# Optimization experiments

Measured on AMD Instinct MI355X. Metric: run time of the kernel, lower is better.

The kernel has to match this reference:

```python
import jax, jax.numpy as jnp
import numpy as np

N = 50000      # nodes
E = 800000     # edges
DIN = 128      # in_channels
H = 128        # hidden_channels
G = 64         # graphs in batch
OUT = 8        # head out_channels


def setup_inputs() -> dict:
    key = jax.random.key(0)
    ks = jax.random.split(key, 12)
    s = 0.1  # weight init scale
    x = jax.random.normal(ks[0], (N, DIN), jnp.float32)
    edge_index = jax.random.randint(ks[1], (2, E), 0, N, dtype=jnp.int64)
    batch = jnp.sort(jax.random.randint(ks[2], (N,), 0, G, dtype=jnp.int64))
    W0 = jax.random.normal(ks[3], (DIN, H), jnp.float32) * s
    b0 = jnp.zeros((H,), jnp.float32)
    W1 = jax.random.normal(ks[4], (H, H), jnp.float32) * s
    b1 = jnp.zeros((H,), jnp.float32)
    W2 = jax.random.normal(ks[5], (H, H), jnp.float32) * s
    b2 = jnp.zeros((H,), jnp.float32)
    Wh = jax.random.normal(ks[6], (H, OUT), jnp.float32) * s
    bh = jnp.zeros((OUT,), jnp.float32)
    return {"x": x, "edge_index": edge_index, "batch": batch,
            "W0": W0, "b0": b0, "W1": W1, "b1": b1, "W2": W2, "b2": b2,
            "Wh": Wh, "bh": bh}


def gcn_conv(x, src, dst, W, b):
    # GCNConv with self-loops and symmetric normalization (PyG defaults).
    h = x @ W                                           # [N, H]
    deg = jnp.zeros((N,), h.dtype).at[dst].add(1.0) + 1.0   # in-degree incl. self-loop
    dinv = jax.lax.rsqrt(deg)                           # deg^{-1/2}
    coef = dinv[src] * dinv[dst]                        # [E]
    agg = jnp.zeros_like(h).at[dst].add(h[src] * coef[:, None])
    # self-loop contribution: dinv[i]^2 * h[i]
    return agg + h * (dinv * dinv)[:, None] + b


def reference(x, edge_index, batch, W0, b0, W1, b1, W2, b2, Wh, bh):
    src, dst = edge_index[0], edge_index[1]
    h = jax.nn.relu(gcn_conv(x, src, dst, W0, b0))
    h = jax.nn.relu(gcn_conv(h, src, dst, W1, b1))
    h = gcn_conv(h, src, dst, W2, b2)                   # last layer: no activation
    # global mean pool over graphs
    sums = jnp.zeros((G, H), h.dtype).at[batch].add(h)
    cnt = jnp.zeros((G,), h.dtype).at[batch].add(1.0)
    pooled = sums / jnp.maximum(cnt, 1.0)[:, None]      # [G, H]
    return pooled @ Wh + bh                             # [G, OUT]
```

## Files before the change

kernel.cpp:

```cpp
#include <hip/hip_runtime.h>

#define N_NODES 50000
#define N_EDGES 800000
#define HD 128
#define NGRAPH 64
#define NOUT 8
#define SLOTS 64

typedef __attribute__((ext_vector_type(8))) short bf8_t;
typedef __attribute__((ext_vector_type(4))) float f4_t;
typedef __attribute__((ext_vector_type(8))) unsigned short us8;

__device__ __forceinline__ unsigned short f2b(float f) {
    unsigned u = __float_as_uint(f);
    u += 0x7fffu + ((u >> 16) & 1u);
    return (unsigned short)(u >> 16);
}
__device__ __forceinline__ float b2f(unsigned short h) {
    return __uint_as_float(((unsigned)h) << 16);
}

__global__ __launch_bounds__(256) void fill1_k(const int* __restrict__ src,
                                               const int* __restrict__ dst,
                                               int* __restrict__ degc,
                                               unsigned short* __restrict__ slots) {
    int e = blockIdx.x * 256 + threadIdx.x;
    if (e >= N_EDGES) return;
    int s = __builtin_nontemporal_load(src + e);
    int d = __builtin_nontemporal_load(dst + e);
    int pos = atomicAdd(&degc[d], 1);
    if (pos < SLOTS)
        slots[(size_t)d * SLOTS + pos] = (unsigned short)s;
}

__global__ __launch_bounds__(256) void cvtw_k(const float* __restrict__ W0,
                                              const float* __restrict__ W1,
                                              const float* __restrict__ W2,
                                              unsigned short* __restrict__ WT) {
    int idx = blockIdx.x * 256 + threadIdx.x;
    if (idx >= 3 * HD * HD) return;
    int w = idx >> 14;
    int rem = idx & 16383;
    int n = rem >> 7;
    int k = rem & 127;
    const float* W = (w == 0) ? W0 : (w == 1) ? W1 : W2;
    WT[(size_t)w * HD * HD + n * HD + k] = f2b(W[k * HD + n]);
}

__global__ __launch_bounds__(256) void mm_f32in_k(const float* __restrict__ X,
                                                  const unsigned short* __restrict__ WT,
                                                  const int* __restrict__ degc,
                                                  unsigned short* __restrict__ Y) {
    const int lane = threadIdx.x & 63;
    const int wave = threadIdx.x >> 6;
    const int r = lane & 15;
    const int q = lane >> 4;
    const int row0 = blockIdx.x * 64 + wave * 16;
    int arow = row0 + r; if (arow >= N_NODES) arow = N_NODES - 1;

    f4_t acc[8];
#pragma unroll
    for (int n = 0; n < 8; ++n) acc[n] = (f4_t){0.f, 0.f, 0.f, 0.f};

#pragma unroll
    for (int kb = 0; kb < 4; ++kb) {
        float4 fa = *(const float4*)(X + (size_t)arow * HD + kb * 32 + q * 8);
        float4 fb = *(const float4*)(X + (size_t)arow * HD + kb * 32 + q * 8 + 4);
        bf8_t a;
        a[0] = (short)f2b(fa.x); a[1] = (short)f2b(fa.y);
        a[2] = (short)f2b(fa.z); a[3] = (short)f2b(fa.w);
        a[4] = (short)f2b(fb.x); a[5] = (short)f2b(fb.y);
        a[6] = (short)f2b(fb.z); a[7] = (short)f2b(fb.w);
#pragma unroll
        for (int n = 0; n < 8; ++n) {
            bf8_t b = *(const bf8_t*)(WT + (size_t)(n * 16 + r) * HD + kb * 32 + q * 8);
            acc[n] = __builtin_amdgcn_mfma_f32_16x16x32_bf16(a, b, acc[n], 0, 0, 0);
        }
    }
    const int orow = row0 + q * 4;
#pragma unroll
    for (int i = 0; i < 4; ++i) {
        int rr = orow + i;
        if (rr < N_NODES) {
            float dv = rsqrtf((float)degc[rr] + 1.0f);
#pragma unroll
            for (int n = 0; n < 8; ++n)
                Y[(size_t)rr * HD + n * 16 + r] = f2b(acc[n][i] * dv);
        }
    }
}

__global__ __launch_bounds__(256) void fusedGM2_k(const unsigned short* __restrict__ T,
                                                  const int* __restrict__ degc,
                                                  const unsigned short* __restrict__ slots,
                                                  const float* __restrict__ bias,
                                                  const unsigned short* __restrict__ WT,
                                                  unsigned short* __restrict__ Y) {
    __shared__ unsigned short hs[16][136];
    const int tid = threadIdx.x;
    const int base = blockIdx.x * 16;

    {
        const int g = tid >> 4;
        const int l = tid & 15;
        const int j8 = l * 8;
        const int i = base + g;
        const int dg = degc[i];
        int dc = dg; if (dc > SLOTS) dc = SLOTS;
        const float di = rsqrtf((float)dg + 1.0f);
        const unsigned short* sl = slots + (size_t)i * SLOTS;

        float a[8];
#pragma unroll
        for (int k = 0; k < 8; ++k) a[k] = 0.f;
        int e = 0;
        for (; e + 15 < dc; e += 16) {
            us8 i0 = *(const us8*)(sl + e);
            us8 i1 = *(const us8*)(sl + e + 8);
            us8 v[16];
#pragma unroll
            for (int u = 0; u < 8; ++u) v[u]     = *(const us8*)(T + (size_t)i0[u] * HD + j8);
#pragma unroll
            for (int u = 0; u < 8; ++u) v[u + 8] = *(const us8*)(T + (size_t)i1[u] * HD + j8);
#pragma unroll
            for (int u = 0; u < 16; ++u) {
#pragma unroll
                for (int k = 0; k < 8; ++k) a[k] += b2f(v[u][k]);
            }
        }
        if (e < dc) {
            us8 i0 = *(const us8*)(sl + e);
            us8 i1 = *(const us8*)(sl + e + 8);
            const unsigned short safe = i0[0];
            int s[16]; float m[16];
#pragma unroll
            for (int u = 0; u < 8; ++u) {
                m[u] = (e + u < dc) ? 1.f : 0.f;
                s[u] = (e + u < dc) ? i0[u] : safe;
            }
#pragma unroll
            for (int u = 0; u < 8; ++u) {
                m[u + 8] = (e + 8 + u < dc) ? 1.f : 0.f;
                s[u + 8] = (e + 8 + u < dc) ? i1[u] : safe;
            }
            us8 v[16];
#pragma unroll
            for (int u = 0; u < 16; ++u) v[u] = *(const us8*)(T + (size_t)s[u] * HD + j8);
#pragma unroll
            for (int u = 0; u < 16; ++u) {
#pragma unroll
                for (int k = 0; k < 8; ++k) a[k] = fmaf(m[u], b2f(v[u][k]), a[k]);
            }
        }
        us8 tv = *(const us8*)(T + (size_t)i * HD + j8);
        float4 bv0 = *(const float4*)(bias + j8);
        float4 bv1 = *(const float4*)(bias + j8 + 4);
        float bb[8] = {bv0.x, bv0.y, bv0.z, bv0.w, bv1.x, bv1.y, bv1.z, bv1.w};
        us8 o;
#pragma unroll
        for (int k = 0; k < 8; ++k) {
            float r = di * (a[k] + b2f(tv[k])) + bb[k];
            r = fmaxf(r, 0.f);
            o[k] = f2b(r);
        }
        *(us8*)(&hs[g][j8]) = o;
    }
    __syncthreads();

    {
        const int lane = tid & 63;
        const int wave = tid >> 6;
        const int r = lane & 15;
        const int q = lane >> 4;
        const int n0 = wave * 2;

        f4_t acc0 = (f4_t){0.f, 0.f, 0.f, 0.f};
        f4_t acc1 = (f4_t){0.f, 0.f, 0.f, 0.f};
#pragma unroll
        for (int kb = 0; kb < 4; ++kb) {
            bf8_t a = *(const bf8_t*)(&hs[r][kb * 32 + q * 8]);
            bf8_t b0 = *(const bf8_t*)(WT + (size_t)(n0 * 16 + r) * HD + kb * 32 + q * 8);
            bf8_t b1 = *(const bf8_t*)(WT + (size_t)(n0 * 16 + 16 + r) * HD + kb * 32 + q * 8);
            acc0 = __builtin_amdgcn_mfma_f32_16x16x32_bf16(a, b0, acc0, 0, 0, 0);
            acc1 = __builtin_amdgcn_mfma_f32_16x16x32_bf16(a, b1, acc1, 0, 0, 0);
        }
#pragma unroll
        for (int i = 0; i < 4; ++i) {
            int rr = base + q * 4 + i;
            float dv = rsqrtf((float)degc[rr] + 1.0f);
            Y[(size_t)rr * HD + n0 * 16 + r]      = f2b(acc0[i] * dv);
            Y[(size_t)rr * HD + n0 * 16 + 16 + r] = f2b(acc1[i] * dv);
        }
    }
}

__global__ __launch_bounds__(256) void gather_k(const unsigned short* __restrict__ T,
                                                const int* __restrict__ degc,
                                                const unsigned short* __restrict__ slots,
                                                const float* __restrict__ b,
                                                unsigned short* __restrict__ out) {
    int i = blockIdx.x * 16 + (threadIdx.x >> 4);
    if (i >= N_NODES) return;
    const int j8 = (threadIdx.x & 15) * 8;
    const int dg = degc[i];
    int dc = dg; if (dc > SLOTS) dc = SLOTS;
    const float di = rsqrtf((float)dg + 1.0f);
    const unsigned short* sl = slots + (size_t)i * SLOTS;

    float a[8];
#pragma unroll
    for (int k = 0; k < 8; ++k) a[k] = 0.f;
    int e = 0;
    for (; e + 15 < dc; e += 16) {
        us8 i0 = *(const us8*)(sl + e);
        us8 i1 = *(const us8*)(sl + e + 8);
        us8 v[16];
#pragma unroll
        for (int u = 0; u < 8; ++u) v[u]     = *(const us8*)(T + (size_t)i0[u] * HD + j8);
#pragma unroll
        for (int u = 0; u < 8; ++u) v[u + 8] = *(const us8*)(T + (size_t)i1[u] * HD + j8);
#pragma unroll
        for (int u = 0; u < 16; ++u) {
#pragma unroll
            for (int k = 0; k < 8; ++k) a[k] += b2f(v[u][k]);
        }
    }
    if (e < dc) {
        us8 i0 = *(const us8*)(sl + e);
        us8 i1 = *(const us8*)(sl + e + 8);
        const unsigned short safe = i0[0];
        int s[16]; float m[16];
#pragma unroll
        for (int u = 0; u < 8; ++u) {
            m[u] = (e + u < dc) ? 1.f : 0.f;
            s[u] = (e + u < dc) ? i0[u] : safe;
        }
#pragma unroll
        for (int u = 0; u < 8; ++u) {
            m[u + 8] = (e + 8 + u < dc) ? 1.f : 0.f;
            s[u + 8] = (e + 8 + u < dc) ? i1[u] : safe;
        }
        us8 v[16];
#pragma unroll
        for (int u = 0; u < 16; ++u) v[u] = *(const us8*)(T + (size_t)s[u] * HD + j8);
#pragma unroll
        for (int u = 0; u < 16; ++u) {
#pragma unroll
            for (int k = 0; k < 8; ++k) a[k] = fmaf(m[u], b2f(v[u][k]), a[k]);
        }
    }
    us8 tv = *(const us8*)(T + (size_t)i * HD + j8);
    float4 bv0 = *(const float4*)(b + j8);
    float4 bv1 = *(const float4*)(b + j8 + 4);
    float bb[8] = {bv0.x, bv0.y, bv0.z, bv0.w, bv1.x, bv1.y, bv1.z, bv1.w};
    us8 o;
#pragma unroll
    for (int k = 0; k < 8; ++k)
        o[k] = f2b(di * (a[k] + b2f(tv[k])) + bb[k]);
    *(us8*)(out + (size_t)i * HD + j8) = o;
}

__global__ __launch_bounds__(256) void pool2_k(const unsigned short* __restrict__ H2,
                                               const int* __restrict__ batch,
                                               float* __restrict__ sums,
                                               float* __restrict__ cnt) {
    const int t = threadIdx.x;
    const int f = t & 127;
    const int half = t >> 7;
    int i0 = blockIdx.x * 128 + half * 64;
    if (i0 >= N_NODES) return;
    int i1 = i0 + 64; if (i1 > N_NODES) i1 = N_NODES;

    int cur = batch[i0];
    float acc = 0.f;
    float c = 0.f;
    for (int i = i0; i < i1; ++i) {
        int g = batch[i];
        if (g != cur) {
            atomicAdd(&sums[cur * HD + f], acc);
            if (f == 0) atomicAdd(&cnt[cur], c);
            acc = 0.f; c = 0.f; cur = g;
        }
        acc += b2f(H2[(size_t)i * HD + f]);
        c += 1.f;
    }
    atomicAdd(&sums[cur * HD + f], acc);
    if (f == 0) atomicAdd(&cnt[cur], c);
}

__global__ __launch_bounds__(512) void head_k(const float* __restrict__ sums,
                                              const float* __restrict__ cnt,
                                              const float* __restrict__ Wh,
                                              const float* __restrict__ bh,
                                              float* __restrict__ out) {
    int t = threadIdx.x;
    int g = t >> 3, o = t & 7;
    float inv = 1.0f / fmaxf(cnt[g], 1.0f);
    float acc = bh[o];
    for (int h = 0; h < HD; ++h)
        acc += sums[g * HD + h] * inv * Wh[h * NOUT + o];
    out[g * NOUT + o] = acc;
}

extern "C" void kernel_launch(void* const* d_in, const int* in_sizes, int n_in,
                              void* d_out, int out_size, void* d_ws, size_t ws_size,
                              hipStream_t stream) {
    const float* x  = (const float*)d_in[0];
    const int*   ei = (const int*)d_in[1];
    const int*   batch = (const int*)d_in[2];
    const float* W0 = (const float*)d_in[3];
    const float* b0 = (const float*)d_in[4];
    const float* W1 = (const float*)d_in[5];
    const float* b1 = (const float*)d_in[6];
    const float* W2 = (const float*)d_in[7];
    const float* b2 = (const float*)d_in[8];
    const float* Wh = (const float*)d_in[9];
    const float* bh = (const float*)d_in[10];
    float* out = (float*)d_out;

    const int* src = ei;
    const int* dst = ei + N_EDGES;

    char* wsb = (char*)d_ws;
    int*            degc  = (int*)(wsb + 0);
    unsigned short* slots = (unsigned short*)(wsb + 200000);
    unsigned short* WT    = (unsigned short*)(wsb + 6600000);
    unsigned short* A     = (unsigned short*)(wsb + 6698304);
    unsigned short* C     = (unsigned short*)(wsb + 19498304);
    float*          sums  = (float*)(wsb + 32298304);
    float*          cnt   = (float*)(wsb + 32331072);

    const int mmGrid = (N_NODES + 63) / 64;
    const int gaGrid = (N_NODES + 15) / 16;

    hipMemsetAsync(degc, 0, N_NODES * sizeof(int), stream);
    fill1_k<<<(N_EDGES + 255) / 256, 256, 0, stream>>>(src, dst, degc, slots);
    cvtw_k<<<(3 * HD * HD + 255) / 256, 256, 0, stream>>>(W0, W1, W2, WT);

    mm_f32in_k<<<mmGrid, 256, 0, stream>>>(x, WT, degc, A);

    fusedGM2_k<<<gaGrid, 256, 0, stream>>>(A, degc, slots, b0, WT + HD * HD, C);

    fusedGM2_k<<<gaGrid, 256, 0, stream>>>(C, degc, slots, b1, WT + 2 * HD * HD, A);

    gather_k<<<gaGrid, 256, 0, stream>>>(A, degc, slots, b2, C);

    hipMemsetAsync(sums, 0, (NGRAPH * HD + NGRAPH) * sizeof(float), stream);
    pool2_k<<<(N_NODES + 127) / 128, 256, 0, stream>>>(C, batch, sums, cnt);
    head_k<<<1, 512, 0, stream>>>(sums, cnt, Wh, bh, out);
}
```

Measured before the change: 305.9 us.

## Merge edge fill with first matmul and fuse final gather with mean pooling

The first-layer matmul now writes unnormalized features, so it no longer depends on degrees and runs in the same launch as the edge-bucketing atomics. The first aggregation therefore applies per-neighbour normalization by reading degc for each neighbour. The last gather writes into shared memory and pools per block with atomics, which removes the write and re-read of the final hidden features and one launch. The cost is extra degc gathers and rsqrt work in layer one, plus more atomic traffic in pooling.

Measured after the change: 347.9 us. 1.14x slower.

```diff
diff --git a/kernel.cpp b/kernel.cpp
--- a/kernel.cpp
+++ b/kernel.cpp
@@ -6,6 +6,8 @@
 #define NGRAPH 64
 #define NOUT 8
 #define SLOTS 64
+#define MMGRID 782
+#define GAGRID 3125
 
 typedef __attribute__((ext_vector_type(8))) short bf8_t;
 typedef __attribute__((ext_vector_type(4))) float f4_t;
@@ -18,19 +20,6 @@
 }
 __device__ __forceinline__ float b2f(unsigned short h) {
     return __uint_as_float(((unsigned)h) << 16);
-}
-
-__global__ __launch_bounds__(256) void fill1_k(const int* __restrict__ src,
-                                               const int* __restrict__ dst,
-                                               int* __restrict__ degc,
-                                               unsigned short* __restrict__ slots) {
-    int e = blockIdx.x * 256 + threadIdx.x;
-    if (e >= N_EDGES) return;
-    int s = __builtin_nontemporal_load(src + e);
-    int d = __builtin_nontemporal_load(dst + e);
-    int pos = atomicAdd(&degc[d], 1);
-    if (pos < SLOTS)
-        slots[(size_t)d * SLOTS + pos] = (unsigned short)s;
 }
 
 __global__ __launch_bounds__(256) void cvtw_k(const float* __restrict__ W0,
@@ -47,45 +36,168 @@
     WT[(size_t)w * HD * HD + n * HD + k] = f2b(W[k * HD + n]);
 }
 
-__global__ __launch_bounds__(256) void mm_f32in_k(const float* __restrict__ X,
-                                                  const unsigned short* __restrict__ WT,
-                                                  const int* __restrict__ degc,
-                                                  unsigned short* __restrict__ Y) {
-    const int lane = threadIdx.x & 63;
-    const int wave = threadIdx.x >> 6;
-    const int r = lane & 15;
-    const int q = lane >> 4;
-    const int row0 = blockIdx.x * 64 + wave * 16;
-    int arow = row0 + r; if (arow >= N_NODES) arow = N_NODES - 1;
-
-    f4_t acc[8];
-#pragma unroll
-    for (int n = 0; n < 8; ++n) acc[n] = (f4_t){0.f, 0.f, 0.f, 0.f};
-
-#pragma unroll
-    for (int kb = 0; kb < 4; ++kb) {
-        float4 fa = *(const float4*)(X + (size_t)arow * HD + kb * 32 + q * 8);
-        float4 fb = *(const float4*)(X + (size_t)arow * HD + kb * 32 + q * 8 + 4);
-        bf8_t a;
-        a[0] = (short)f2b(fa.x); a[1] = (short)f2b(fa.y);
-        a[2] = (short)f2b(fa.z); a[3] = (short)f2b(fa.w);
-        a[4] = (short)f2b(fb.x); a[5] = (short)f2b(fb.y);
-        a[6] = (short)f2b(fb.z); a[7] = (short)f2b(fb.w);
-#pragma unroll
-        for (int n = 0; n < 8; ++n) {
-            bf8_t b = *(const bf8_t*)(WT + (size_t)(n * 16 + r) * HD + kb * 32 + q * 8);
-            acc[n] = __builtin_amdgcn_mfma_f32_16x16x32_bf16(a, b, acc[n], 0, 0, 0);
-        }
-    }
-    const int orow = row0 + q * 4;
-#pragma unroll
-    for (int i = 0; i < 4; ++i) {
-        int rr = orow + i;
-        if (rr < N_NODES) {
+__global__ __launch_bounds__(256) void fillmm_k(const float* __restrict__ X,
+                                                const unsigned short* __restrict__ WT,
+                                                const int* __restrict__ src,
+                                                const int* __restrict__ dst,
+                                                int* __restrict__ degc,
+                                                unsigned short* __restrict__ slots,
+                                                unsigned short* __restrict__ Y) {
+    if (blockIdx.x < MMGRID) {
+        const int lane = threadIdx.x & 63;
+        const int wave = threadIdx.x >> 6;
+        const int r = lane & 15;
+        const int q = lane >> 4;
+        const int row0 = blockIdx.x * 64 + wave * 16;
+        int arow = row0 + r; if (arow >= N_NODES) arow = N_NODES - 1;
+
+        f4_t acc[8];
+#pragma unroll
+        for (int n = 0; n < 8; ++n) acc[n] = (f4_t){0.f, 0.f, 0.f, 0.f};
+
+#pragma unroll
+        for (int kb = 0; kb < 4; ++kb) {
+            float4 fa = *(const float4*)(X + (size_t)arow * HD + kb * 32 + q * 8);
+            float4 fb = *(const float4*)(X + (size_t)arow * HD + kb * 32 + q * 8 + 4);
+            bf8_t a;
+            a[0] = (short)f2b(fa.x); a[1] = (short)f2b(fa.y);
+            a[2] = (short)f2b(fa.z); a[3] = (short)f2b(fa.w);
+            a[4] = (short)f2b(fb.x); a[5] = (short)f2b(fb.y);
+            a[6] = (short)f2b(fb.z); a[7] = (short)f2b(fb.w);
+#pragma unroll
+            for (int n = 0; n < 8; ++n) {
+                bf8_t b = *(const bf8_t*)(WT + (size_t)(n * 16 + r) * HD + kb * 32 + q * 8);
+                acc[n] = __builtin_amdgcn_mfma_f32_16x16x32_bf16(a, b, acc[n], 0, 0, 0);
+            }
+        }
+        const int orow = row0 + q * 4;
+#pragma unroll
+        for (int i = 0; i < 4; ++i) {
+            int rr = orow + i;
+            if (rr < N_NODES) {
+#pragma unroll
+                for (int n = 0; n < 8; ++n)
+                    Y[(size_t)rr * HD + n * 16 + r] = f2b(acc[n][i]);
+            }
+        }
+        return;
+    }
+    int e = (blockIdx.x - MMGRID) * 256 + threadIdx.x;
+    if (e >= N_EDGES) return;
+    int s = __builtin_nontemporal_load(src + e);
+    int d = __builtin_nontemporal_load(dst + e);
+    int pos = atomicAdd(&degc[d], 1);
+    if (pos < SLOTS)
+        slots[(size_t)d * SLOTS + pos] = (unsigned short)s;
+}
+
+__global__ __launch_bounds__(256) void fusedGM2c_k(const unsigned short* __restrict__ T,
+                                                   const int* __restrict__ degc,
+                                                   const unsigned short* __restrict__ slots,
+                                                   const float* __restrict__ bias,
+                                                   const unsigned short* __restrict__ WT,
+                                                   unsigned short* __restrict__ Y) {
+    __shared__ unsigned short hs[16][136];
+    const int tid = threadIdx.x;
+    const int base = blockIdx.x * 16;
+
+    {
+        const int g = tid >> 4;
+        const int l = tid & 15;
+        const int j8 = l * 8;
+        const int i = base + g;
+        const int dg = degc[i];
+        int dc = dg; if (dc > SLOTS) dc = SLOTS;
+        const float di = rsqrtf((float)dg + 1.0f);
+        const unsigned short* sl = slots + (size_t)i * SLOTS;
+
+        float a[8];
+#pragma unroll
+        for (int k = 0; k < 8; ++k) a[k] = 0.f;
+        int e = 0;
+        for (; e + 15 < dc; e += 16) {
+            us8 i0 = *(const us8*)(sl + e);
+            us8 i1 = *(const us8*)(sl + e + 8);
+            float c[16];
+#pragma unroll
+            for (int u = 0; u < 8; ++u) c[u]     = rsqrtf((float)degc[i0[u]] + 1.0f);
+#pragma unroll
+            for (int u = 0; u < 8; ++u) c[u + 8] = rsqrtf((float)degc[i1[u]] + 1.0f);
+            us8 v[16];
+#pragma unroll
+            for (int u = 0; u < 8; ++u) v[u]     = *(const us8*)(T + (size_t)i0[u] * HD + j8);
+#pragma unroll
+            for (int u = 0; u < 8; ++u) v[u + 8] = *(const us8*)(T + (size_t)i1[u] * HD + j8);
+#pragma unroll
+            for (int u = 0; u < 16; ++u) {
+#pragma unroll
+                for (int k = 0; k < 8; ++k) a[k] = fmaf(c[u], b2f(v[u][k]), a[k]);
+            }
+        }
+        if (e < dc) {
+            us8 i0 = *(const us8*)(sl + e);
+            us8 i1 = *(const us8*)(sl + e + 8);
+            const unsigned short safe = i0[0];
+            int s[16]; float mc[16];
+#pragma unroll
+            for (int u = 0; u < 8; ++u) {
+                bool ok = (e + u < dc);
+                s[u] = ok ? i0[u] : safe;
+                mc[u] = ok ? rsqrtf((float)degc[s[u]] + 1.0f) : 0.f;
+            }
+#pragma unroll
+            for (int u = 0; u < 8; ++u) {
+                bool ok = (e + 8 + u < dc);
+                s[u + 8] = ok ? i1[u] : safe;
+                mc[u + 8] = ok ? rsqrtf((float)degc[s[u + 8]] + 1.0f) : 0.f;
+            }
+            us8 v[16];
+#pragma unroll
+            for (int u = 0; u < 16; ++u) v[u] = *(const us8*)(T + (size_t)s[u] * HD + j8);
+#pragma unroll
+            for (int u = 0; u < 16; ++u) {
+#pragma unroll
+                for (int k = 0; k < 8; ++k) a[k] = fmaf(mc[u], b2f(v[u][k]), a[k]);
+            }
+        }
+        us8 tv = *(const us8*)(T + (size_t)i * HD + j8);
+        float4 bv0 = *(const float4*)(bias + j8);
+        float4 bv1 = *(const float4*)(bias + j8 + 4);
+        float bb[8] = {bv0.x, bv0.y, bv0.z, bv0.w, bv1.x, bv1.y, bv1.z, bv1.w};
+        us8 o;
+#pragma unroll
+        for (int k = 0; k < 8; ++k) {
+            float r = di * (a[k] + di * b2f(tv[k])) + bb[k];
+            r = fmaxf(r, 0.f);
+            o[k] = f2b(r);
+        }
+        *(us8*)(&hs[g][j8]) = o;
+    }
+    __syncthreads();
+
+    {
+        const int lane = tid & 63;
+        const int wave = tid >> 6;
+        const int r = lane & 15;
+        const int q = lane >> 4;
+        const int n0 = wave * 2;
+
+        f4_t acc0 = (f4_t){0.f, 0.f, 0.f, 0.f};
+        f4_t acc1 = (f4_t){0.f, 0.f, 0.f, 0.f};
+#pragma unroll
+        for (int kb = 0; kb < 4; ++kb) {
+            bf8_t a = *(const bf8_t*)(&hs[r][kb * 32 + q * 8]);
+            bf8_t b0 = *(const bf8_t*)(WT + (size_t)(n0 * 16 + r) * HD + kb * 32 + q * 8);
+            bf8_t b1 = *(const bf8_t*)(WT + (size_t)(n0 * 16 + 16 + r) * HD + kb * 32 + q * 8);
+            acc0 = __builtin_amdgcn_mfma_f32_16x16x32_bf16(a, b0, acc0, 0, 0, 0);
+            acc1 = __builtin_amdgcn_mfma_f32_16x16x32_bf16(a, b1, acc1, 0, 0, 0);
+        }
+#pragma unroll
+        for (int i = 0; i < 4; ++i) {
+            int rr = base + q * 4 + i;
             float dv = rsqrtf((float)degc[rr] + 1.0f);
-#pragma unroll
-            for (int n = 0; n < 8; ++n)
-                Y[(size_t)rr * HD + n * 16 + r] = f2b(acc[n][i] * dv);
+            Y[(size_t)rr * HD + n0 * 16 + r]      = f2b(acc0[i] * dv);
+            Y[(size_t)rr * HD + n0 * 16 + 16 + r] = f2b(acc1[i] * dv);
         }
     }
 }
@@ -194,98 +306,99 @@
     }
 }
 
-__global__ __launch_bounds__(256) void gather_k(const unsigned short* __restrict__ T,
-                                                const int* __restrict__ degc,
-                                                const unsigned short* __restrict__ slots,
-                                                const float* __restrict__ b,
-                                                unsigned short* __restrict__ out) {
-    int i = blockIdx.x * 16 + (threadIdx.x >> 4);
-    if (i >= N_NODES) return;
-    const int j8 = (threadIdx.x & 15) * 8;
-    const int dg = degc[i];
-    int dc = dg; if (dc > SLOTS) dc = SLOTS;
-    const float di = rsqrtf((float)dg + 1.0f);
-    const unsigned short* sl = slots + (size_t)i * SLOTS;
-
-    float a[8];
-#pragma unroll
-    for (int k = 0; k < 8; ++k) a[k] = 0.f;
-    int e = 0;
-    for (; e + 15 < dc; e += 16) {
-        us8 i0 = *(const us8*)(sl + e);
-        us8 i1 = *(const us8*)(sl + e + 8);
-        us8 v[16];
-#pragma unroll
-        for (int u = 0; u < 8; ++u) v[u]     = *(const us8*)(T + (size_t)i0[u] * HD + j8);
-#pragma unroll
-        for (int u = 0; u < 8; ++u) v[u + 8] = *(const us8*)(T + (size_t)i1[u] * HD + j8);
-#pragma unroll
-        for (int u = 0; u < 16; ++u) {
-#pragma unroll
-            for (int k = 0; k < 8; ++k) a[k] += b2f(v[u][k]);
-        }
-    }
-    if (e < dc) {
-        us8 i0 = *(const us8*)(sl + e);
-        us8 i1 = *(const us8*)(sl + e + 8);
-        const unsigned short safe = i0[0];
-        int s[16]; float m[16];
-#pragma unroll
-        for (int u = 0; u < 8; ++u) {
-            m[u] = (e + u < dc) ? 1.f : 0.f;
-            s[u] = (e + u < dc) ? i0[u] : safe;
-        }
-#pragma unroll
-        for (int u = 0; u < 8; ++u) {
-            m[u + 8] = (e + 8 + u < dc) ? 1.f : 0.f;
-            s[u + 8] = (e + 8 + u < dc) ? i1[u] : safe;
-        }
-        us8 v[16];
-#pragma unroll
-        for (int u = 0; u < 16; ++u) v[u] = *(const us8*)(T + (size_t)s[u] * HD + j8);
-#pragma unroll
-        for (int u = 0; u < 16; ++u) {
-#pragma unroll
-            for (int k = 0; k < 8; ++k) a[k] = fmaf(m[u], b2f(v[u][k]), a[k]);
-        }
-    }
-    us8 tv = *(const us8*)(T + (size_t)i * HD + j8);
-    float4 bv0 = *(const float4*)(b + j8);
-    float4 bv1 = *(const float4*)(b + j8 + 4);
-    float bb[8] = {bv0.x, bv0.y, bv0.z, bv0.w, bv1.x, bv1.y, bv1.z, bv1.w};
-    us8 o;
-#pragma unroll
-    for (int k = 0; k < 8; ++k)
-        o[k] = f2b(di * (a[k] + b2f(tv[k])) + bb[k]);
-    *(us8*)(out + (size_t)i * HD + j8) = o;
-}
-
-__global__ __launch_bounds__(256) void pool2_k(const unsigned short* __restrict__ H2,
+__global__ __launch_bounds__(256) void gpool_k(const unsigned short* __restrict__ T,
+                                               const int* __restrict__ degc,
+                                               const unsigned short* __restrict__ slots,
+                                               const float* __restrict__ b,
                                                const int* __restrict__ batch,
                                                float* __restrict__ sums,
                                                float* __restrict__ cnt) {
-    const int t = threadIdx.x;
-    const int f = t & 127;
-    const int half = t >> 7;
-    int i0 = blockIdx.x * 128 + half * 64;
-    if (i0 >= N_NODES) return;
-    int i1 = i0 + 64; if (i1 > N_NODES) i1 = N_NODES;
-
-    int cur = batch[i0];
-    float acc = 0.f;
-    float c = 0.f;
-    for (int i = i0; i < i1; ++i) {
-        int g = batch[i];
-        if (g != cur) {
-            atomicAdd(&sums[cur * HD + f], acc);
-            if (f == 0) atomicAdd(&cnt[cur], c);
-            acc = 0.f; c = 0.f; cur = g;
-        }
-        acc += b2f(H2[(size_t)i * HD + f]);
-        c += 1.f;
-    }
-    atomicAdd(&sums[cur * HD + f], acc);
-    if (f == 0) atomicAdd(&cnt[cur], c);
+    __shared__ float hsf[16][128];
+    const int tid = threadIdx.x;
+    const int base = blockIdx.x * 16;
+
+    {
+        const int g = tid >> 4;
+        const int j8 = (tid & 15) * 8;
+        const int i = base + g;
+        const int dg = degc[i];
+        int dc = dg; if (dc > SLOTS) dc = SLOTS;
+        const float di = rsqrtf((float)dg + 1.0f);
+        const unsigned short* sl = slots + (size_t)i * SLOTS;
+
+        float a[8];
+#pragma unroll
+        for (int k = 0; k < 8; ++k) a[k] = 0.f;
+        int e = 0;
+        for (; e + 15 < dc; e += 16) {
+            us8 i0 = *(const us8*)(sl + e);
+            us8 i1 = *(const us8*)(sl + e + 8);
+            us8 v[16];
+#pragma unroll
+            for (int u = 0; u < 8; ++u) v[u]     = *(const us8*)(T + (size_t)i0[u] * HD + j8);
+#pragma unroll
+            for (int u = 0; u < 8; ++u) v[u + 8] = *(const us8*)(T + (size_t)i1[u] * HD + j8);
+#pragma unroll
+            for (int u = 0; u < 16; ++u) {
+#pragma unroll
+                for (int k = 0; k < 8; ++k) a[k] += b2f(v[u][k]);
+            }
+        }
+        if (e < dc) {
+            us8 i0 = *(const us8*)(sl + e);
+            us8 i1 = *(const us8*)(sl + e + 8);
+            const unsigned short safe = i0[0];
+            int s[16]; float m[16];
+#pragma unroll
+            for (int u = 0; u < 8; ++u) {
+                m[u] = (e + u < dc) ? 1.f : 0.f;
+                s[u] = (e + u < dc) ? i0[u] : safe;
+            }
+#pragma unroll
+            for (int u = 0; u < 8; ++u) {
+                m[u + 8] = (e + 8 + u < dc) ? 1.f : 0.f;
+                s[u + 8] = (e + 8 + u < dc) ? i1[u] : safe;
+            }
+            us8 v[16];
+#pragma unroll
+            for (int u = 0; u < 16; ++u) v[u] = *(const us8*)(T + (size_t)s[u] * HD + j8);
+#pragma unroll
+            for (int u = 0; u < 16; ++u) {
+#pragma unroll
+                for (int k = 0; k < 8; ++k) a[k] = fmaf(m[u], b2f(v[u][k]), a[k]);
+            }
+        }
+        us8 tv = *(const us8*)(T + (size_t)i * HD + j8);
+        float4 bv0 = *(const float4*)(b + j8);
+        float4 bv1 = *(const float4*)(b + j8 + 4);
+        float bb[8] = {bv0.x, bv0.y, bv0.z, bv0.w, bv1.x, bv1.y, bv1.z, bv1.w};
+#pragma unroll
+        for (int k = 0; k < 8; ++k)
+            hsf[g][j8 + k] = di * (a[k] + b2f(tv[k])) + bb[k];
+    }
+    __syncthreads();
+
+    {
+        const int f = tid & 127;
+        const int half = tid >> 7;
+        const int r0 = half * 8;
+        int cur = batch[base + r0];
+        float acc = 0.f;
+        float c = 0.f;
+#pragma unroll
+        for (int r = r0; r < r0 + 8; ++r) {
+            int gg = batch[base + r];
+            if (gg != cur) {
+                atomicAdd(&sums[cur * HD + f], acc);
+                if (f == 0) atomicAdd(&cnt[cur], c);
+                acc = 0.f; c = 0.f; cur = gg;
+            }
+            acc += hsf[r][f];
+            c += 1.f;
+        }
+        atomicAdd(&sums[cur * HD + f], acc);
+        if (f == 0) atomicAdd(&cnt[cur], c);
+    }
 }
 
 __global__ __launch_bounds__(512) void head_k(const float* __restrict__ sums,
@@ -330,22 +443,19 @@
     float*          sums  = (float*)(wsb + 32298304);
     float*          cnt   = (float*)(wsb + 32331072);
 
-    const int mmGrid = (N_NODES + 63) / 64;
-    const int gaGrid = (N_NODES + 15) / 16;
+    const int fillGrid = (N_EDGES + 255) / 256;
 
     hipMemsetAsync(degc, 0, N_NODES * sizeof(int), stream);
-    fill1_k<<<(N_EDGES + 255) / 256, 256, 0, stream>>>(src, dst, degc, slots);
+    hipMemsetAsync(sums, 0, (NGRAPH * HD + NGRAPH) * sizeof(float), stream);
     cvtw_k<<<(3 * HD * HD + 255) / 256, 256, 0, stream>>>(W0, W1, W2, WT);
 
-    mm_f32in_k<<<mmGrid, 256, 0, stream>>>(x, WT, degc, A);
-
-    fusedGM2_k<<<gaGrid, 256, 0, stream>>>(A, degc, slots, b0, WT + HD * HD, C);
-
-    fusedGM2_k<<<gaGrid, 256, 0, stream>>>(C, degc, slots, b1, WT + 2 * HD * HD, A);
-
-    gather_k<<<gaGrid, 256, 0, stream>>>(A, degc, slots, b2, C);
-
-    hipMemsetAsync(sums, 0, (NGRAPH * HD + NGRAPH) * sizeof(float), stream);
-    pool2_k<<<(N_NODES + 127) / 128, 256, 0, stream>>>(C, batch, sums, cnt);
+    fillmm_k<<<MMGRID + fillGrid, 256, 0, stream>>>(x, WT, src, dst, degc, slots, A);
+
+    fusedGM2c_k<<<GAGRID, 256, 0, stream>>>(A, degc, slots, b0, WT + HD * HD, C);
+
+    fusedGM2_k<<<GAGRID, 256, 0, stream>>>(C, degc, slots, b1, WT + 2 * HD * HD, A);
+
+    gpool_k<<<GAGRID, 256, 0, stream>>>(A, degc, slots, b2, batch, sums, cnt);
+
     head_k<<<1, 512, 0, stream>>>(sums, cnt, Wh, bh, out);
 }
```

## Fuse final gather with mean pooling and fold memsets into weight conversion

Applied to the files above, without the earlier changes.

The last-layer gather now writes its fp32 results to shared memory and pools them into per-graph sums with atomics in the same kernel. This removes the bf16 H2 round trip through global memory and one kernel launch. The degree, sums and count zeroing moves from two hipMemsetAsync calls into the weight-conversion kernel, which now runs before fill1. The x loads in the first matmul become nontemporal. The pooling step now issues atomics per 8-row chunk instead of per 64-row span, which raises atomic traffic on the 64x128 sums array.

After: 317.6 us. 3.9% more time.

```diff
diff --git a/kernel.cpp b/kernel.cpp
--- a/kernel.cpp
+++ b/kernel.cpp
@@ -6,6 +6,7 @@
 #define NGRAPH 64
 #define NOUT 8
 #define SLOTS 64
+#define GAGRID 3125
 
 typedef __attribute__((ext_vector_type(8))) short bf8_t;
 typedef __attribute__((ext_vector_type(4))) float f4_t;
@@ -18,6 +19,27 @@
 }
 __device__ __forceinline__ float b2f(unsigned short h) {
     return __uint_as_float(((unsigned)h) << 16);
+}
+
+__global__ __launch_bounds__(256) void cvtw_k(const float* __restrict__ W0,
+                                              const float* __restrict__ W1,
+                                              const float* __restrict__ W2,
+                                              unsigned short* __restrict__ WT,
+                                              int* __restrict__ degc,
+                                              float* __restrict__ sums,
+                                              float* __restrict__ cnt) {
+    int idx = blockIdx.x * 256 + threadIdx.x;
+    if (idx < 3 * HD * HD) {
+        int w = idx >> 14;
+        int rem = idx & 16383;
+        int n = rem >> 7;
+        int k = rem & 127;
+        const float* W = (w == 0) ? W0 : (w == 1) ? W1 : W2;
+        WT[(size_t)w * HD * HD + n * HD + k] = f2b(W[k * HD + n]);
+    }
+    if (idx < N_NODES) degc[idx] = 0;
+    if (idx < NGRAPH * HD) sums[idx] = 0.f;
+    if (idx < NGRAPH) cnt[idx] = 0.f;
 }
 
 __global__ __launch_bounds__(256) void fill1_k(const int* __restrict__ src,
@@ -33,20 +55,6 @@
         slots[(size_t)d * SLOTS + pos] = (unsigned short)s;
 }
 
-__global__ __launch_bounds__(256) void cvtw_k(const float* __restrict__ W0,
-                                              const float* __restrict__ W1,
-                                              const float* __restrict__ W2,
-                                              unsigned short* __restrict__ WT) {
-    int idx = blockIdx.x * 256 + threadIdx.x;
-    if (idx >= 3 * HD * HD) return;
-    int w = idx >> 14;
-    int rem = idx & 16383;
-    int n = rem >> 7;
-    int k = rem & 127;
-    const float* W = (w == 0) ? W0 : (w == 1) ? W1 : W2;
-    WT[(size_t)w * HD * HD + n * HD + k] = f2b(W[k * HD + n]);
-}
-
 __global__ __launch_bounds__(256) void mm_f32in_k(const float* __restrict__ X,
                                                   const unsigned short* __restrict__ WT,
                                                   const int* __restrict__ degc,
@@ -64,13 +72,13 @@
 
 #pragma unroll
     for (int kb = 0; kb < 4; ++kb) {
-        float4 fa = *(const float4*)(X + (size_t)arow * HD + kb * 32 + q * 8);
-        float4 fb = *(const float4*)(X + (size_t)arow * HD + kb * 32 + q * 8 + 4);
+        f4_t fa = __builtin_nontemporal_load((const f4_t*)(X + (size_t)arow * HD + kb * 32 + q * 8));
+        f4_t fb = __builtin_nontemporal_load((const f4_t*)(X + (size_t)arow * HD + kb * 32 + q * 8 + 4));
         bf8_t a;
-        a[0] = (short)f2b(fa.x); a[1] = (short)f2b(fa.y);
-        a[2] = (short)f2b(fa.z); a[3] = (short)f2b(fa.w);
-        a[4] = (short)f2b(fb.x); a[5] = (short)f2b(fb.y);
-        a[6] = (short)f2b(fb.z); a[7] = (short)f2b(fb.w);
+        a[0] = (short)f2b(fa[0]); a[1] = (short)f2b(fa[1]);
+        a[2] = (short)f2b(fa[2]); a[3] = (short)f2b(fa[3]);
+        a[4] = (short)f2b(fb[0]); a[5] = (short)f2b(fb[1]);
+        a[6] = (short)f2b(fb[2]); a[7] = (short)f2b(fb[3]);
 #pragma unroll
         for (int n = 0; n < 8; ++n) {
             bf8_t b = *(const bf8_t*)(WT + (size_t)(n * 16 + r) * HD + kb * 32 + q * 8);
@@ -194,98 +202,99 @@
     }
 }
 
-__global__ __launch_bounds__(256) void gather_k(const unsigned short* __restrict__ T,
-                                                const int* __restrict__ degc,
-                                                const unsigned short* __restrict__ slots,
-                                                const float* __restrict__ b,
-                                                unsigned short* __restrict__ out) {
-    int i = blockIdx.x * 16 + (threadIdx.x >> 4);
-    if (i >= N_NODES) return;
-    const int j8 = (threadIdx.x & 15) * 8;
-    const int dg = degc[i];
-    int dc = dg; if (dc > SLOTS) dc = SLOTS;
-    const float di = rsqrtf((float)dg + 1.0f);
-    const unsigned short* sl = slots + (size_t)i * SLOTS;
-
-    float a[8];
-#pragma unroll
-    for (int k = 0; k < 8; ++k) a[k] = 0.f;
-    int e = 0;
-    for (; e + 15 < dc; e += 16) {
-        us8 i0 = *(const us8*)(sl + e);
-        us8 i1 = *(const us8*)(sl + e + 8);
-        us8 v[16];
-#pragma unroll
-        for (int u = 0; u < 8; ++u) v[u]     = *(const us8*)(T + (size_t)i0[u] * HD + j8);
-#pragma unroll
-        for (int u = 0; u < 8; ++u) v[u + 8] = *(const us8*)(T + (size_t)i1[u] * HD + j8);
-#pragma unroll
-        for (int u = 0; u < 16; ++u) {
-#pragma unroll
-            for (int k = 0; k < 8; ++k) a[k] += b2f(v[u][k]);
-        }
-    }
-    if (e < dc) {
-        us8 i0 = *(const us8*)(sl + e);
-        us8 i1 = *(const us8*)(sl + e + 8);
-        const unsigned short safe = i0[0];
-        int s[16]; float m[16];
-#pragma unroll
-        for (int u = 0; u < 8; ++u) {
-            m[u] = (e + u < dc) ? 1.f : 0.f;
-            s[u] = (e + u < dc) ? i0[u] : safe;
-        }
-#pragma unroll
-        for (int u = 0; u < 8; ++u) {
-            m[u + 8] = (e + 8 + u < dc) ? 1.f : 0.f;
-            s[u + 8] = (e + 8 + u < dc) ? i1[u] : safe;
-        }
-        us8 v[16];
-#pragma unroll
-        for (int u = 0; u < 16; ++u) v[u] = *(const us8*)(T + (size_t)s[u] * HD + j8);
-#pragma unroll
-        for (int u = 0; u < 16; ++u) {
-#pragma unroll
-            for (int k = 0; k < 8; ++k) a[k] = fmaf(m[u], b2f(v[u][k]), a[k]);
-        }
-    }
-    us8 tv = *(const us8*)(T + (size_t)i * HD + j8);
-    float4 bv0 = *(const float4*)(b + j8);
-    float4 bv1 = *(const float4*)(b + j8 + 4);
-    float bb[8] = {bv0.x, bv0.y, bv0.z, bv0.w, bv1.x, bv1.y, bv1.z, bv1.w};
-    us8 o;
-#pragma unroll
-    for (int k = 0; k < 8; ++k)
-        o[k] = f2b(di * (a[k] + b2f(tv[k])) + bb[k]);
-    *(us8*)(out + (size_t)i * HD + j8) = o;
-}
-
-__global__ __launch_bounds__(256) void pool2_k(const unsigned short* __restrict__ H2,
+__global__ __launch_bounds__(256) void gpool_k(const unsigned short* __restrict__ T,
+                                               const int* __restrict__ degc,
+                                               const unsigned short* __restrict__ slots,
+                                               const float* __restrict__ b,
                                                const int* __restrict__ batch,
                                                float* __restrict__ sums,
                                                float* __restrict__ cnt) {
-    const int t = threadIdx.x;
-    const int f = t & 127;
-    const int half = t >> 7;
-    int i0 = blockIdx.x * 128 + half * 64;
-    if (i0 >= N_NODES) return;
-    int i1 = i0 + 64; if (i1 > N_NODES) i1 = N_NODES;
-
-    int cur = batch[i0];
-    float acc = 0.f;
-    float c = 0.f;
-    for (int i = i0; i < i1; ++i) {
-        int g = batch[i];
-        if (g != cur) {
-            atomicAdd(&sums[cur * HD + f], acc);
-            if (f == 0) atomicAdd(&cnt[cur], c);
-            acc = 0.f; c = 0.f; cur = g;
-        }
-        acc += b2f(H2[(size_t)i * HD + f]);
-        c += 1.f;
-    }
-    atomicAdd(&sums[cur * HD + f], acc);
-    if (f == 0) atomicAdd(&cnt[cur], c);
+    __shared__ float hsf[16][128];
+    const int tid = threadIdx.x;
+    const int base = blockIdx.x * 16;
+
+    {
+        const int g = tid >> 4;
+        const int j8 = (tid & 15) * 8;
+        const int i = base + g;
+        const int dg = degc[i];
+        int dc = dg; if (dc > SLOTS) dc = SLOTS;
+        const float di = rsqrtf((float)dg + 1.0f);
+        const unsigned short* sl = slots + (size_t)i * SLOTS;
+
+        float a[8];
+#pragma unroll
+        for (int k = 0; k < 8; ++k) a[k] = 0.f;
+        int e = 0;
+        for (; e + 15 < dc; e += 16) {
+            us8 i0 = *(const us8*)(sl + e);
+            us8 i1 = *(const us8*)(sl + e + 8);
+            us8 v[16];
+#pragma unroll
+            for (int u = 0; u < 8; ++u) v[u]     = *(const us8*)(T + (size_t)i0[u] * HD + j8);
+#pragma unroll
+            for (int u = 0; u < 8; ++u) v[u + 8] = *(const us8*)(T + (size_t)i1[u] * HD + j8);
+#pragma unroll
+            for (int u = 0; u < 16; ++u) {
+#pragma unroll
+                for (int k = 0; k < 8; ++k) a[k] += b2f(v[u][k]);
+            }
+        }
+        if (e < dc) {
+            us8 i0 = *(const us8*)(sl + e);
+            us8 i1 = *(const us8*)(sl + e + 8);
+            const unsigned short safe = i0[0];
+            int s[16]; float m[16];
+#pragma unroll
+            for (int u = 0; u < 8; ++u) {
+                m[u] = (e + u < dc) ? 1.f : 0.f;
+                s[u] = (e + u < dc) ? i0[u] : safe;
+            }
+#pragma unroll
+            for (int u = 0; u < 8; ++u) {
+                m[u + 8] = (e + 8 + u < dc) ? 1.f : 0.f;
+                s[u + 8] = (e + 8 + u < dc) ? i1[u] : safe;
+            }
+            us8 v[16];
+#pragma unroll
+            for (int u = 0; u < 16; ++u) v[u] = *(const us8*)(T + (size_t)s[u] * HD + j8);
+#pragma unroll
+            for (int u = 0; u < 16; ++u) {
+#pragma unroll
+                for (int k = 0; k < 8; ++k) a[k] = fmaf(m[u], b2f(v[u][k]), a[k]);
+            }
+        }
+        us8 tv = *(const us8*)(T + (size_t)i * HD + j8);
+        float4 bv0 = *(const float4*)(b + j8);
+        float4 bv1 = *(const float4*)(b + j8 + 4);
+        float bb[8] = {bv0.x, bv0.y, bv0.z, bv0.w, bv1.x, bv1.y, bv1.z, bv1.w};
+#pragma unroll
+        for (int k = 0; k < 8; ++k)
+            hsf[g][j8 + k] = di * (a[k] + b2f(tv[k])) + bb[k];
+    }
+    __syncthreads();
+
+    {
+        const int f = tid & 127;
+        const int half = tid >> 7;
+        const int r0 = half * 8;
+        int cur = batch[base + r0];
+        float acc = 0.f;
+        float c = 0.f;
+#pragma unroll
+        for (int r = r0; r < r0 + 8; ++r) {
+            int gg = batch[base + r];
+            if (gg != cur) {
+                atomicAdd(&sums[cur * HD + f], acc);
+                if (f == 0) atomicAdd(&cnt[cur], c);
+                acc = 0.f; c = 0.f; cur = gg;
+            }
+            acc += hsf[r][f];
+            c += 1.f;
+        }
+        atomicAdd(&sums[cur * HD + f], acc);
+        if (f == 0) atomicAdd(&cnt[cur], c);
+    }
 }
 
 __global__ __launch_bounds__(512) void head_k(const float* __restrict__ sums,
@@ -331,21 +340,18 @@
     float*          cnt   = (float*)(wsb + 32331072);
 
     const int mmGrid = (N_NODES + 63) / 64;
-    const int gaGrid = (N_NODES + 15) / 16;
-
-    hipMemsetAsync(degc, 0, N_NODES * sizeof(int), stream);
+
+    cvtw_k<<<(N_NODES + 255) / 256, 256, 0, stream>>>(W0, W1, W2, WT, degc, sums, cnt);
+
     fill1_k<<<(N_EDGES + 255) / 256, 256, 0, stream>>>(src, dst, degc, slots);
-    cvtw_k<<<(3 * HD * HD + 255) / 256, 256, 0, stream>>>(W0, W1, W2, WT);
 
     mm_f32in_k<<<mmGrid, 256, 0, stream>>>(x, WT, degc, A);
 
-    fusedGM2_k<<<gaGrid, 256, 0, stream>>>(A, degc, slots, b0, WT + HD * HD, C);
-
-    fusedGM2_k<<<gaGrid, 256, 0, stream>>>(C, degc, slots, b1, WT + 2 * HD * HD, A);
-
-    gather_k<<<gaGrid, 256, 0, stream>>>(A, degc, slots, b2, C);
-
-    hipMemsetAsync(sums, 0, (NGRAPH * HD + NGRAPH) * sizeof(float), stream);
-    pool2_k<<<(N_NODES + 127) / 128, 256, 0, stream>>>(C, batch, sums, cnt);
+    fusedGM2_k<<<GAGRID, 256, 0, stream>>>(A, degc, slots, b0, WT + HD * HD, C);
+
+    fusedGM2_k<<<GAGRID, 256, 0, stream>>>(C, degc, slots, b1, WT + 2 * HD * HD, A);
+
+    gpool_k<<<GAGRID, 256, 0, stream>>>(A, degc, slots, b2, batch, sums, cnt);
+
     head_k<<<1, 512, 0, stream>>>(sums, cnt, Wh, bh, out);
 }
```

## Partition edge slot fill by destination group and fold memsets into weight conversion

Applied to the files above, without the earlier changes.

The CSR-like slot fill now runs in chunks of edges, each processed by 8 blocks. Each block handles only the destinations whose (d>>4)&7 bucket matches its own, which localizes atomics and slot writes per block and likely improves cache locality on the scattered writes. In exchange, every dst element is read eight times. The two hipMemsetAsync calls are removed, and their zeroing of degc, sums and cnt moves into the weight-conversion kernel, which cuts launch overhead. The x loads in the first matmul become nontemporal.

After: 299.0 us. -2.2%, faster.

```diff
diff --git a/kernel.cpp b/kernel.cpp
--- a/kernel.cpp
+++ b/kernel.cpp
@@ -6,6 +6,8 @@
 #define NGRAPH 64
 #define NOUT 8
 #define SLOTS 64
+#define GAGRID 3125
+#define EPB 2048
 
 typedef __attribute__((ext_vector_type(8))) short bf8_t;
 typedef __attribute__((ext_vector_type(4))) float f4_t;
@@ -20,31 +22,44 @@
     return __uint_as_float(((unsigned)h) << 16);
 }
 
-__global__ __launch_bounds__(256) void fill1_k(const int* __restrict__ src,
+__global__ __launch_bounds__(256) void cvtw_k(const float* __restrict__ W0,
+                                              const float* __restrict__ W1,
+                                              const float* __restrict__ W2,
+                                              unsigned short* __restrict__ WT,
+                                              int* __restrict__ degc,
+                                              float* __restrict__ sums,
+                                              float* __restrict__ cnt) {
+    int idx = blockIdx.x * 256 + threadIdx.x;
+    if (idx < 3 * HD * HD) {
+        int w = idx >> 14;
+        int rem = idx & 16383;
+        int n = rem >> 7;
+        int k = rem & 127;
+        const float* W = (w == 0) ? W0 : (w == 1) ? W1 : W2;
+        WT[(size_t)w * HD * HD + n * HD + k] = f2b(W[k * HD + n]);
+    }
+    if (idx < N_NODES) degc[idx] = 0;
+    if (idx < NGRAPH * HD) sums[idx] = 0.f;
+    if (idx < NGRAPH) cnt[idx] = 0.f;
+}
+
+__global__ __launch_bounds__(256) void fillx_k(const int* __restrict__ src,
                                                const int* __restrict__ dst,
                                                int* __restrict__ degc,
                                                unsigned short* __restrict__ slots) {
-    int e = blockIdx.x * 256 + threadIdx.x;
-    if (e >= N_EDGES) return;
-    int s = __builtin_nontemporal_load(src + e);
-    int d = __builtin_nontemporal_load(dst + e);
-    int pos = atomicAdd(&degc[d], 1);
-    if (pos < SLOTS)
-        slots[(size_t)d * SLOTS + pos] = (unsigned short)s;
-}
-
-__global__ __launch_bounds__(256) void cvtw_k(const float* __restrict__ W0,
-                                              const float* __restrict__ W1,
-                                              const float* __restrict__ W2,
-                                              unsigned short* __restrict__ WT) {
-    int idx = blockIdx.x * 256 + threadIdx.x;
-    if (idx >= 3 * HD * HD) return;
-    int w = idx >> 14;
-    int rem = idx & 16383;
-    int n = rem >> 7;
-    int k = rem & 127;
-    const float* W = (w == 0) ? W0 : (w == 1) ? W1 : W2;
-    WT[(size_t)w * HD * HD + n * HD + k] = f2b(W[k * HD + n]);
+    const int p = blockIdx.x & 7;
+    const int c = blockIdx.x >> 3;
+    const int e0 = c * EPB;
+    int e1 = e0 + EPB; if (e1 > N_EDGES) e1 = N_EDGES;
+    for (int e = e0 + threadIdx.x; e < e1; e += 256) {
+        int d = dst[e];
+        if (((d >> 4) & 7) == p) {
+            int s = src[e];
+            int pos = atomicAdd(&degc[d], 1);
+            if (pos < SLOTS)
+                slots[(size_t)d * SLOTS + pos] = (unsigned short)s;
+        }
+    }
 }
 
 __global__ __launch_bounds__(256) void mm_f32in_k(const float* __restrict__ X,
@@ -64,13 +79,13 @@
 
 #pragma unroll
     for (int kb = 0; kb < 4; ++kb) {
-        float4 fa = *(const float4*)(X + (size_t)arow * HD + kb * 32 + q * 8);
-        float4 fb = *(const float4*)(X + (size_t)arow * HD + kb * 32 + q * 8 + 4);
+        f4_t fa = __builtin_nontemporal_load((const f4_t*)(X + (size_t)arow * HD + kb * 32 + q * 8));
+        f4_t fb = __builtin_nontemporal_load((const f4_t*)(X + (size_t)arow * HD + kb * 32 + q * 8 + 4));
         bf8_t a;
-        a[0] = (short)f2b(fa.x); a[1] = (short)f2b(fa.y);
-        a[2] = (short)f2b(fa.z); a[3] = (short)f2b(fa.w);
-        a[4] = (short)f2b(fb.x); a[5] = (short)f2b(fb.y);
-        a[6] = (short)f2b(fb.z); a[7] = (short)f2b(fb.w);
+        a[0] = (short)f2b(fa[0]); a[1] = (short)f2b(fa[1]);
+        a[2] = (short)f2b(fa[2]); a[3] = (short)f2b(fa[3]);
+        a[4] = (short)f2b(fb[0]); a[5] = (short)f2b(fb[1]);
+        a[6] = (short)f2b(fb[2]); a[7] = (short)f2b(fb[3]);
 #pragma unroll
         for (int n = 0; n < 8; ++n) {
             bf8_t b = *(const bf8_t*)(WT + (size_t)(n * 16 + r) * HD + kb * 32 + q * 8);
@@ -331,21 +346,20 @@
     float*          cnt   = (float*)(wsb + 32331072);
 
     const int mmGrid = (N_NODES + 63) / 64;
-    const int gaGrid = (N_NODES + 15) / 16;
-
-    hipMemsetAsync(degc, 0, N_NODES * sizeof(int), stream);
-    fill1_k<<<(N_EDGES + 255) / 256, 256, 0, stream>>>(src, dst, degc, slots);
-    cvtw_k<<<(3 * HD * HD + 255) / 256, 256, 0, stream>>>(W0, W1, W2, WT);
+    const int fillxGrid = ((N_EDGES + EPB - 1) / EPB) * 8;
+
+    cvtw_k<<<(N_NODES + 255) / 256, 256, 0, stream>>>(W0, W1, W2, WT, degc, sums, cnt);
+
+    fillx_k<<<fillxGrid, 256, 0, stream>>>(src, dst, degc, slots);
 
     mm_f32in_k<<<mmGrid, 256, 0, stream>>>(x, WT, degc, A);
 
-    fusedGM2_k<<<gaGrid, 256, 0, stream>>>(A, degc, slots, b0, WT + HD * HD, C);
-
-    fusedGM2_k<<<gaGrid, 256, 0, stream>>>(C, degc, slots, b1, WT + 2 * HD * HD, A);
-
-    gather_k<<<gaGrid, 256, 0, stream>>>(A, degc, slots, b2, C);
-
-    hipMemsetAsync(sums, 0, (NGRAPH * HD + NGRAPH) * sizeof(float), stream);
+    fusedGM2_k<<<GAGRID, 256, 0, stream>>>(A, degc, slots, b0, WT + HD * HD, C);
+
+    fusedGM2_k<<<GAGRID, 256, 0, stream>>>(C, degc, slots, b1, WT + 2 * HD * HD, A);
+
+    gather_k<<<GAGRID, 256, 0, stream>>>(A, degc, slots, b2, C);
+
     pool2_k<<<(N_NODES + 127) / 128, 256, 0, stream>>>(C, batch, sums, cnt);
     head_k<<<1, 512, 0, stream>>>(sums, cnt, Wh, bh, out);
 }
```
